# Performance work log

Measured on AMD Instinct MI355X. Metric: run time of the kernel, lower is better.

Reference implementation:

```python
import jax, jax.numpy as jnp
import numpy as np

U = 100000  # num_users
I = 100000  # num_items
D = 64      # dims
L = 50      # seq_L


def setup_inputs() -> dict:
    key = jax.random.key(0)
    ks = jax.random.split(key, 12)
    B, T = 4096, 100
    inp = {
        "user_ids": jax.random.randint(ks[0], (B,), 0, U),
        "item_seq_ids": jax.random.randint(ks[1], (B, L), 0, I),
        "target_item_ids": jax.random.randint(ks[2], (B, T), 0, I),
        # embedding tables (normal init)
        "user_table": jax.random.normal(ks[3], (U, D), jnp.float32) * 0.01,
        "item_table": jax.random.normal(ks[4], (I, D), jnp.float32) * 0.01,
        "W2_table": jax.random.normal(ks[5], (I, D), jnp.float32) * 0.01,
        "b2_table": jnp.zeros((I, 1), jnp.float32),
        # feature gates: Linear(dims, dims), he_uniform weight, zero bias
        "fg_item_W": jax.random.uniform(ks[6], (D, D), jnp.float32, -1.0, 1.0) * np.sqrt(6.0 / D),
        "fg_item_b": jnp.zeros((D,), jnp.float32),
        "fg_user_W": jax.random.uniform(ks[7], (D, D), jnp.float32, -1.0, 1.0) * np.sqrt(6.0 / D),
        "fg_user_b": jnp.zeros((D,), jnp.float32),
        # instance gates: xavier_uniform
        "inst_gate_item": jax.random.uniform(ks[8], (D, 1), jnp.float32, -1.0, 1.0) * np.sqrt(6.0 / (D + 1)),
        "inst_gate_user": jax.random.uniform(ks[9], (D, L), jnp.float32, -1.0, 1.0) * np.sqrt(6.0 / (D + L)),
    }
    return inp


def _forward_user(user_emb, item_embs, fg_item_W, fg_item_b, fg_user_W, fg_user_b,
                  inst_gate_item, inst_gate_user):
    # user_emb: [B,D], item_embs: [B,L,D]
    gate = jax.nn.sigmoid(
        item_embs @ fg_item_W.T + fg_item_b
        + (user_emb @ fg_user_W.T + fg_user_b)[:, None, :]
    )  # [B,L,D]
    gated = item_embs * gate  # [B,L,D]
    term1 = jnp.einsum("bld,d->bl", gated, inst_gate_item[:, 0])
    term2 = user_emb @ inst_gate_user  # [B,L]
    inst = jax.nn.sigmoid(term1 + term2)  # [B,L]
    union = jnp.sum(gated * inst[:, :, None], axis=1)  # [B,D]
    union = union / jnp.sum(inst, axis=1, keepdims=True)
    return union


def reference(user_ids, item_seq_ids, target_item_ids, user_table, item_table,
              W2_table, b2_table, fg_item_W, fg_item_b, fg_user_W, fg_user_b,
              inst_gate_item, inst_gate_user):
    item_embs = item_table[item_seq_ids]      # [B,L,D]
    user_emb = user_table[user_ids]           # [B,D]
    union = _forward_user(user_emb, item_embs, fg_item_W, fg_item_b,
                          fg_user_W, fg_user_b, inst_gate_item, inst_gate_user)
    w2 = W2_table[target_item_ids]            # [B,T,D]
    b2 = b2_table[target_item_ids][..., 0]    # [B,T]
    res = b2 + jnp.einsum("btd,bd->bt", w2, user_emb)
    res = res + jnp.einsum("bd,btd->bt", union, w2)
    # rel_score: bmm(item_embs, w2^T) summed over L == contract item_embs summed over L with w2
    res = res + jnp.einsum("bd,btd->bt", jnp.sum(item_embs, axis=1), w2)
    return res
```

## Files before the change

kernel.cpp:

```cpp
#include <hip/hip_runtime.h>

#define DD 64
#define LL 50
#define NB 4096
#define NT 100

typedef __attribute__((ext_vector_type(8))) __bf16 bf16x8;
typedef __attribute__((ext_vector_type(4))) float f32x4;

__device__ __forceinline__ float sigmoidf_(float x) {
    return 1.0f / (1.0f + __expf(-x));
}
__device__ __forceinline__ unsigned pack_bf16(float hi, float lo) {
    union { float f; unsigned u; } a, b;
    a.f = hi; b.f = lo;
    return ((a.u + 0x8000u) & 0xffff0000u) | ((b.u + 0x8000u) >> 16);
}
__device__ __forceinline__ uint4 cvt8u(const float* f) {
    uint4 r;
    r.x = pack_bf16(f[1], f[0]);
    r.y = pack_bf16(f[3], f[2]);
    r.z = pack_bf16(f[5], f[4]);
    r.w = pack_bf16(f[7], f[6]);
    return r;
}
__device__ __forceinline__ bf16x8 cvt8(const float* f) {
    return __builtin_bit_cast(bf16x8, cvt8u(f));
}
__device__ __forceinline__ void glds16(const float* g, float* l) {
    __builtin_amdgcn_global_load_lds(
        (const __attribute__((address_space(1))) void*)g,
        (__attribute__((address_space(3))) void*)l, 16, 0, 0);
}
__device__ __forceinline__ void glds4(const float* g, float* l) {
    __builtin_amdgcn_global_load_lds(
        (const __attribute__((address_space(1))) void*)g,
        (__attribute__((address_space(3))) void*)l, 4, 0, 0);
}

__global__ __launch_bounds__(64) void k0_user(
    const int* __restrict__ uid_g, const float* __restrict__ user_table,
    const float* __restrict__ Wu, const float* __restrict__ bu,
    const float* __restrict__ bi, const float* __restrict__ igu,
    const float* __restrict__ Wi,
    float* __restrict__ ufg_ws, float* __restrict__ t2_ws,
    unsigned short* __restrict__ wiB_ws)
{
    if (blockIdx.x == 256) {
        const int n = threadIdx.x;
        float tmp[64];
#pragma unroll
        for (int c4 = 0; c4 < 16; c4++)
            *(float4*)&tmp[c4 * 4] = *(const float4*)(Wi + n * DD + c4 * 4);
#pragma unroll
        for (int ch = 0; ch < 8; ch++)
            *(uint4*)(wiB_ws + n * DD + ch * 8) = cvt8u(tmp + ch * 8);
        return;
    }

    const int lane = threadIdx.x;
    const int c = lane & 15, q = lane >> 4;
    const int uid = uid_g[blockIdx.x * 16 + c];
    const float* urow = user_table + (size_t)uid * DD;

    bf16x8 af[2];
#pragma unroll
    for (int kf = 0; kf < 2; kf++) {
        float tmp[8];
        *(float4*)&tmp[0] = *(const float4*)(urow + kf * 32 + q * 8);
        *(float4*)&tmp[4] = *(const float4*)(urow + kf * 32 + q * 8 + 4);
        af[kf] = cvt8(tmp);
    }

#pragma unroll
    for (int ni = 0; ni < 8; ni++) {
        f32x4 a = {0.f, 0.f, 0.f, 0.f};
#pragma unroll
        for (int kf = 0; kf < 2; kf++) {
            const int k0 = kf * 32 + q * 8;
            float tmp[8];
            if (ni < 4) {
                const float* src = Wu + (ni * 16 + c) * DD + k0;
                *(float4*)&tmp[0] = *(const float4*)src;
                *(float4*)&tmp[4] = *(const float4*)(src + 4);
            } else {
                const int l = ni * 16 + c - 64;
#pragma unroll
                for (int j = 0; j < 8; j++)
                    tmp[j] = (l < LL) ? igu[(k0 + j) * LL + l] : 0.f;
            }
            a = __builtin_amdgcn_mfma_f32_16x16x32_bf16(af[kf], cvt8(tmp), a, 0, 0, 0);
        }
        const int n = ni * 16 + c;
#pragma unroll
        for (int reg = 0; reg < 4; reg++) {
            const int bo = blockIdx.x * 16 + q * 4 + reg;
            if (n < DD)           ufg_ws[bo * DD + n] = a[reg] + bu[n] + bi[n];
            else if (n < DD + LL) t2_ws[bo * DD + (n - DD)] = a[reg];
        }
    }
}

__global__ __launch_bounds__(64) void k1_union(
    const int* __restrict__ uid_g, const int* __restrict__ iid_g,
    const float* __restrict__ user_table, const float* __restrict__ item_table,
    const unsigned short* __restrict__ wiB, const float* __restrict__ igi,
    const float* __restrict__ ufg_ws, const float* __restrict__ t2_ws,
    float* __restrict__ v_ws)
{
    const int lane = threadIdx.x;
    const int c = lane & 15, q = lane >> 4;
    const int b = blockIdx.x;

    __shared__ __align__(16) float sE[52 * DD + DD];
    float* sT = sE + 52 * DD;

    const int* iidp = iid_g + b * LL;
    int ids[13];
#pragma unroll
    for (int s = 0; s < 13; s++) {
        const int r = 4 * s + (lane >> 4);
        ids[s] = iidp[r < LL ? r : LL - 1];
    }

#pragma unroll
    for (int s = 0; s < 13; s++) {
        const int r = 4 * s + (lane >> 4);
        const int j = (lane & 15) ^ (r & 7);
        glds16(item_table + (size_t)ids[s] * DD + j * 4, sE + s * 256);
    }
    glds4(t2_ws + b * DD + (lane < LL ? lane : LL - 1), sT);

    bf16x8 wb[4][2];
#pragma unroll
    for (int ni = 0; ni < 4; ni++)
#pragma unroll
        for (int kf = 0; kf < 2; kf++)
            wb[ni][kf] = __builtin_bit_cast(bf16x8,
                *(const uint4*)(wiB + (ni * 16 + c) * DD + kf * 32 + q * 8));

    float ufg4[4], igi4[4];
#pragma unroll
    for (int ni = 0; ni < 4; ni++) {
        ufg4[ni] = ufg_ws[b * DD + ni * 16 + c];
        igi4[ni] = igi[ni * 16 + c];
    }
    const int uid = uid_g[b];
    const float u = user_table[(size_t)uid * DD + lane];

    __syncthreads();

    bf16x8 ea[4][2];
#pragma unroll
    for (int mi = 0; mi < 4; mi++) {
        const int row = mi * 16 + c;
        const int rr = (row < LL) ? row : 0;
        const float* rowp = sE + rr * DD;
        const int s7 = rr & 7;
#pragma unroll
        for (int kf = 0; kf < 2; kf++) {
            float tmp[8];
            const int ch0 = (kf * 8 + 2 * q) ^ s7;
            const int ch1 = (kf * 8 + 2 * q + 1) ^ s7;
            *(float4*)&tmp[0] = *(const float4*)(rowp + ch0 * 4);
            *(float4*)&tmp[4] = *(const float4*)(rowp + ch1 * 4);
            if (row >= LL) {
#pragma unroll
                for (int i = 0; i < 8; i++) tmp[i] = 0.f;
            }
            ea[mi][kf] = cvt8(tmp);
        }
    }

    float unum[4] = {0.f, 0.f, 0.f, 0.f};
    float sip[4]  = {0.f, 0.f, 0.f, 0.f};
    float isum = 0.f;

#pragma unroll
    for (int mi = 0; mi < 4; mi++) {
        f32x4 acc[4];
#pragma unroll
        for (int ni = 0; ni < 4; ni++) {
            f32x4 a = {0.f, 0.f, 0.f, 0.f};
            a = __builtin_amdgcn_mfma_f32_16x16x32_bf16(ea[mi][0], wb[ni][0], a, 0, 0, 0);
            a = __builtin_amdgcn_mfma_f32_16x16x32_bf16(ea[mi][1], wb[ni][1], a, 0, 0, 0);
            acc[ni] = a;
        }
        float gated[4][4], inst_r[4];
#pragma unroll
        for (int reg = 0; reg < 4; reg++) {
            const int l = mi * 16 + q * 4 + reg;
            const int valid = (l < LL);
            const int lr = valid ? l : 0;
            const int s7 = lr & 7;
            float t1 = 0.f;
#pragma unroll
            for (int ni = 0; ni < 4; ni++) {
                const int phys = (4 * ni + (c >> 2)) ^ s7;
                const float ev = sE[lr * DD + phys * 4 + (c & 3)];
                const float e = valid ? ev : 0.f;
                const float g = sigmoidf_(acc[ni][reg] + ufg4[ni]);
                const float gd = e * g;
                gated[reg][ni] = gd;
                t1 += gd * igi4[ni];
                sip[ni] += e;
            }
            t1 += __shfl_xor(t1, 1); t1 += __shfl_xor(t1, 2);
            t1 += __shfl_xor(t1, 4); t1 += __shfl_xor(t1, 8);
            inst_r[reg] = valid ? sigmoidf_(t1 + sT[lr]) : 0.f;
        }
#pragma unroll
        for (int reg = 0; reg < 4; reg++) {
            isum += inst_r[reg];
#pragma unroll
            for (int ni = 0; ni < 4; ni++)
                unum[ni] += gated[reg][ni] * inst_r[reg];
        }
    }

#pragma unroll
    for (int ni = 0; ni < 4; ni++) {
        unum[ni] += __shfl_xor(unum[ni], 16); unum[ni] += __shfl_xor(unum[ni], 32);
        sip[ni]  += __shfl_xor(sip[ni], 16);  sip[ni]  += __shfl_xor(sip[ni], 32);
    }
    isum += __shfl_xor(isum, 16); isum += __shfl_xor(isum, 32);

    const float un = (q == 0) ? unum[0] : (q == 1) ? unum[1] : (q == 2) ? unum[2] : unum[3];
    const float si = (q == 0) ? sip[0]  : (q == 1) ? sip[1]  : (q == 2) ? sip[2]  : sip[3];
    v_ws[b * DD + lane] = u + un / isum + si;
}

__global__ __launch_bounds__(256) void k2_score(
    const int* __restrict__ tgt_g, const float* __restrict__ W2,
    const float* __restrict__ b2, const float* __restrict__ v_ws,
    float* __restrict__ out)
{
    const int b = blockIdx.x;
    const int tid = threadIdx.x;
    __shared__ float sv[DD];
    __shared__ int sids[112];
    __shared__ float sout[112];

    if (tid < DD) sv[tid] = v_ws[b * DD + tid];
    if (tid < 112) {
        const int t = (tid < NT) ? tid : NT - 1;
        sids[tid] = tgt_g[b * NT + t];
    }
    __syncthreads();

    const int j = tid & 15, g = tid >> 4;
    float4 vr = *(const float4*)&sv[j * 4];

    int id[7];
#pragma unroll
    for (int i = 0; i < 7; i++) id[i] = sids[i * 16 + g];
    float4 wv[7];
#pragma unroll
    for (int i = 0; i < 7; i++)
        wv[i] = *(const float4*)(W2 + (size_t)id[i] * DD + j * 4);
    float bb[7];
#pragma unroll
    for (int i = 0; i < 7; i++) bb[i] = b2[id[i]];

#pragma unroll
    for (int i = 0; i < 7; i++) {
        float s = wv[i].x * vr.x + wv[i].y * vr.y + wv[i].z * vr.z + wv[i].w * vr.w;
        s += __shfl_xor(s, 1); s += __shfl_xor(s, 2);
        s += __shfl_xor(s, 4); s += __shfl_xor(s, 8);
        if (j == 0) sout[i * 16 + g] = s + bb[i];
    }
    __syncthreads();
    if (tid < NT) out[b * NT + tid] = sout[tid];
}

extern "C" void kernel_launch(void* const* d_in, const int* in_sizes, int n_in,
                              void* d_out, int out_size, void* d_ws, size_t ws_size,
                              hipStream_t stream)
{
    const int* user_ids        = (const int*)d_in[0];
    const int* item_seq_ids    = (const int*)d_in[1];
    const int* target_item_ids = (const int*)d_in[2];
    const float* user_tab      = (const float*)d_in[3];
    const float* item_tab      = (const float*)d_in[4];
    const float* W2_tab        = (const float*)d_in[5];
    const float* b2_tab        = (const float*)d_in[6];
    const float* fg_item_W     = (const float*)d_in[7];
    const float* fg_item_b     = (const float*)d_in[8];
    const float* fg_user_W     = (const float*)d_in[9];
    const float* fg_user_b     = (const float*)d_in[10];
    const float* igi           = (const float*)d_in[11];
    const float* igu           = (const float*)d_in[12];
    float* out = (float*)d_out;

    float* ufg_ws = (float*)d_ws;
    float* t2_ws  = ufg_ws + NB * DD;
    float* v_ws   = t2_ws + NB * DD;
    unsigned short* wiB_ws = (unsigned short*)(v_ws + NB * DD);

    k0_user<<<257, 64, 0, stream>>>(user_ids, user_tab, fg_user_W, fg_user_b,
                                    fg_item_b, igu, fg_item_W,
                                    ufg_ws, t2_ws, wiB_ws);
    k1_union<<<NB, 64, 0, stream>>>(user_ids, item_seq_ids, user_tab, item_tab,
                                    wiB_ws, igi, ufg_ws, t2_ws, v_ws);
    k2_score<<<NB, 256, 0, stream>>>(target_item_ids, W2_tab, b2_tab, v_ws, out);
}
```

Baseline: 160.5 us.

## Fuse union and scoring kernels, split L rows across four waves

Merges the union kernel and the scoring kernel into one 256-thread block per batch row. Each of the four waves handles a 16-row slice of the item sequence, and partial sums are reduced through shared memory. W2 rows and b2 values are prefetched into LDS with async global-to-LDS loads so they overlap with the gating math. This removes the v_ws round-trip through global memory and one kernel launch. k0 now uses two waves per block. The cost is much higher LDS use per block (about 45KB), which may limit occupancy, plus extra block-level syncs.

```diff
diff --git a/kernel.cpp b/kernel.cpp
--- a/kernel.cpp
+++ b/kernel.cpp
@@ -38,7 +38,7 @@
         (__attribute__((address_space(3))) void*)l, 4, 0, 0);
 }
 
-__global__ __launch_bounds__(64) void k0_user(
+__global__ __launch_bounds__(128) void k0_user(
     const int* __restrict__ uid_g, const float* __restrict__ user_table,
     const float* __restrict__ Wu, const float* __restrict__ bu,
     const float* __restrict__ bi, const float* __restrict__ igu,
@@ -47,6 +47,7 @@
     unsigned short* __restrict__ wiB_ws)
 {
     if (blockIdx.x == 256) {
+        if (threadIdx.x >= 64) return;
         const int n = threadIdx.x;
         float tmp[64];
 #pragma unroll
@@ -58,7 +59,8 @@
         return;
     }
 
-    const int lane = threadIdx.x;
+    const int lane = threadIdx.x & 63;
+    const int wv = threadIdx.x >> 6;
     const int c = lane & 15, q = lane >> 4;
     const int uid = uid_g[blockIdx.x * 16 + c];
     const float* urow = user_table + (size_t)uid * DD;
@@ -73,7 +75,8 @@
     }
 
 #pragma unroll
-    for (int ni = 0; ni < 8; ni++) {
+    for (int ni0 = 0; ni0 < 4; ni0++) {
+        const int ni = wv * 4 + ni0;
         f32x4 a = {0.f, 0.f, 0.f, 0.f};
 #pragma unroll
         for (int kf = 0; kf < 2; kf++) {
@@ -101,35 +104,82 @@
     }
 }
 
-__global__ __launch_bounds__(64) void k1_union(
+__global__ __launch_bounds__(256) void k1_fused(
     const int* __restrict__ uid_g, const int* __restrict__ iid_g,
+    const int* __restrict__ tgt_g,
     const float* __restrict__ user_table, const float* __restrict__ item_table,
+    const float* __restrict__ W2, const float* __restrict__ b2,
     const unsigned short* __restrict__ wiB, const float* __restrict__ igi,
     const float* __restrict__ ufg_ws, const float* __restrict__ t2_ws,
-    float* __restrict__ v_ws)
+    float* __restrict__ out)
 {
-    const int lane = threadIdx.x;
+    const int tid = threadIdx.x;
+    const int lane = tid & 63;
+    const int w = tid >> 6;
     const int c = lane & 15, q = lane >> 4;
     const int b = blockIdx.x;
 
-    __shared__ __align__(16) float sE[52 * DD + DD];
-    float* sT = sE + 52 * DD;
+    __shared__ __align__(16) float sE[52 * DD];
+    __shared__ __align__(16) float sW[112 * DD];
+    __shared__ __align__(16) float sT[DD];
+    __shared__ __align__(16) float sB[128];
+    __shared__ __align__(16) float sU[4 * DD];
+    __shared__ __align__(16) float sS[4 * DD];
+    __shared__ float sI[4];
+    __shared__ __align__(16) float sV[DD];
+    __shared__ float sOut[112];
 
     const int* iidp = iid_g + b * LL;
-    int ids[13];
-#pragma unroll
-    for (int s = 0; s < 13; s++) {
+    const int* tgtp = tgt_g + b * NT;
+
+    int iid3[3];
+#pragma unroll
+    for (int k = 0; k < 3; k++) {
+        const int s = w + 4 * k;
         const int r = 4 * s + (lane >> 4);
-        ids[s] = iidp[r < LL ? r : LL - 1];
-    }
-
-#pragma unroll
-    for (int s = 0; s < 13; s++) {
+        iid3[k] = iidp[r < LL ? r : LL - 1];
+    }
+    int iid12 = 0;
+    if (w == 0) {
+        const int r = 48 + (lane >> 4);
+        iid12 = iidp[r < LL ? r : LL - 1];
+    }
+#pragma unroll
+    for (int k = 0; k < 3; k++) {
+        const int s = w + 4 * k;
         const int r = 4 * s + (lane >> 4);
-        const int j = (lane & 15) ^ (r & 7);
-        glds16(item_table + (size_t)ids[s] * DD + j * 4, sE + s * 256);
-    }
-    glds4(t2_ws + b * DD + (lane < LL ? lane : LL - 1), sT);
+        const int j2 = (lane & 15) ^ (r & 7);
+        glds16(item_table + (size_t)iid3[k] * DD + j2 * 4, sE + s * 256);
+    }
+    if (w == 0) {
+        const int r = 48 + (lane >> 4);
+        const int j2 = (lane & 15) ^ (r & 7);
+        glds16(item_table + (size_t)iid12 * DD + j2 * 4, sE + 12 * 256);
+    }
+
+    int tids6[6];
+#pragma unroll
+    for (int i = 0; i < 6; i++) {
+        const int s2 = w + 4 * i;
+        tids6[i] = tgtp[4 * s2 + (lane >> 4)];
+    }
+    int tid24 = 0;
+    if (w == 0) tid24 = tgtp[96 + (lane >> 4)];
+#pragma unroll
+    for (int i = 0; i < 6; i++) {
+        const int s2 = w + 4 * i;
+        glds16(W2 + (size_t)tids6[i] * DD + (lane & 15) * 4, sW + s2 * 256);
+    }
+    if (w == 0)
+        glds16(W2 + (size_t)tid24 * DD + (lane & 15) * 4, sW + 24 * 256);
+
+    if (w < 2) {
+        const int sl = w * 64 + lane;
+        const int tb = sl < NT ? sl : NT - 1;
+        glds4(b2 + tgtp[tb], sB + w * 64);
+    }
+    if (w == 1)
+        glds4(t2_ws + b * DD + (lane < LL ? lane : LL - 1), sT);
 
     bf16x8 wb[4][2];
 #pragma unroll
@@ -145,15 +195,17 @@
         ufg4[ni] = ufg_ws[b * DD + ni * 16 + c];
         igi4[ni] = igi[ni * 16 + c];
     }
-    const int uid = uid_g[b];
-    const float u = user_table[(size_t)uid * DD + lane];
+    float u = 0.f;
+    if (w == 0) {
+        const int uid = uid_g[b];
+        u = user_table[(size_t)uid * DD + lane];
+    }
 
     __syncthreads();
 
-    bf16x8 ea[4][2];
-#pragma unroll
-    for (int mi = 0; mi < 4; mi++) {
-        const int row = mi * 16 + c;
+    bf16x8 ea[2];
+    {
+        const int row = w * 16 + c;
         const int rr = (row < LL) ? row : 0;
         const float* rowp = sE + rr * DD;
         const int s7 = rr & 7;
@@ -168,28 +220,26 @@
 #pragma unroll
                 for (int i = 0; i < 8; i++) tmp[i] = 0.f;
             }
-            ea[mi][kf] = cvt8(tmp);
+            ea[kf] = cvt8(tmp);
         }
     }
 
     float unum[4] = {0.f, 0.f, 0.f, 0.f};
     float sip[4]  = {0.f, 0.f, 0.f, 0.f};
     float isum = 0.f;
-
-#pragma unroll
-    for (int mi = 0; mi < 4; mi++) {
+    {
         f32x4 acc[4];
 #pragma unroll
         for (int ni = 0; ni < 4; ni++) {
             f32x4 a = {0.f, 0.f, 0.f, 0.f};
-            a = __builtin_amdgcn_mfma_f32_16x16x32_bf16(ea[mi][0], wb[ni][0], a, 0, 0, 0);
-            a = __builtin_amdgcn_mfma_f32_16x16x32_bf16(ea[mi][1], wb[ni][1], a, 0, 0, 0);
+            a = __builtin_amdgcn_mfma_f32_16x16x32_bf16(ea[0], wb[ni][0], a, 0, 0, 0);
+            a = __builtin_amdgcn_mfma_f32_16x16x32_bf16(ea[1], wb[ni][1], a, 0, 0, 0);
             acc[ni] = a;
         }
         float gated[4][4], inst_r[4];
 #pragma unroll
         for (int reg = 0; reg < 4; reg++) {
-            const int l = mi * 16 + q * 4 + reg;
+            const int l = w * 16 + q * 4 + reg;
             const int valid = (l < LL);
             const int lr = valid ? l : 0;
             const int s7 = lr & 7;
@@ -227,50 +277,32 @@
 
     const float un = (q == 0) ? unum[0] : (q == 1) ? unum[1] : (q == 2) ? unum[2] : unum[3];
     const float si = (q == 0) ? sip[0]  : (q == 1) ? sip[1]  : (q == 2) ? sip[2]  : sip[3];
-    v_ws[b * DD + lane] = u + un / isum + si;
-}
-
-__global__ __launch_bounds__(256) void k2_score(
-    const int* __restrict__ tgt_g, const float* __restrict__ W2,
-    const float* __restrict__ b2, const float* __restrict__ v_ws,
-    float* __restrict__ out)
-{
-    const int b = blockIdx.x;
-    const int tid = threadIdx.x;
-    __shared__ float sv[DD];
-    __shared__ int sids[112];
-    __shared__ float sout[112];
-
-    if (tid < DD) sv[tid] = v_ws[b * DD + tid];
-    if (tid < 112) {
-        const int t = (tid < NT) ? tid : NT - 1;
-        sids[tid] = tgt_g[b * NT + t];
-    }
+    sU[w * DD + lane] = un;
+    sS[w * DD + lane] = si;
+    if (lane == 0) sI[w] = isum;
     __syncthreads();
 
-    const int j = tid & 15, g = tid >> 4;
-    float4 vr = *(const float4*)&sv[j * 4];
-
-    int id[7];
-#pragma unroll
-    for (int i = 0; i < 7; i++) id[i] = sids[i * 16 + g];
-    float4 wv[7];
-#pragma unroll
-    for (int i = 0; i < 7; i++)
-        wv[i] = *(const float4*)(W2 + (size_t)id[i] * DD + j * 4);
-    float bb[7];
-#pragma unroll
-    for (int i = 0; i < 7; i++) bb[i] = b2[id[i]];
-
+    if (w == 0) {
+        const float unt = sU[lane] + sU[DD + lane] + sU[2 * DD + lane] + sU[3 * DD + lane];
+        const float sit = sS[lane] + sS[DD + lane] + sS[2 * DD + lane] + sS[3 * DD + lane];
+        const float ist = sI[0] + sI[1] + sI[2] + sI[3];
+        sV[lane] = u + unt / ist + sit;
+    }
+    __syncthreads();
+
+    const int j = tid & 15, gg = tid >> 4;
+    const float4 vr = *(const float4*)&sV[j * 4];
 #pragma unroll
     for (int i = 0; i < 7; i++) {
-        float s = wv[i].x * vr.x + wv[i].y * vr.y + wv[i].z * vr.z + wv[i].w * vr.w;
+        const int ts = i * 16 + gg;
+        const float4 wvv = *(const float4*)&sW[ts * DD + j * 4];
+        float s = wvv.x * vr.x + wvv.y * vr.y + wvv.z * vr.z + wvv.w * vr.w;
         s += __shfl_xor(s, 1); s += __shfl_xor(s, 2);
         s += __shfl_xor(s, 4); s += __shfl_xor(s, 8);
-        if (j == 0) sout[i * 16 + g] = s + bb[i];
+        if (j == 0 && ts < NT) sOut[ts] = s + sB[ts];
     }
     __syncthreads();
-    if (tid < NT) out[b * NT + tid] = sout[tid];
+    if (tid < NT) out[b * NT + tid] = sOut[tid];
 }
 
 extern "C" void kernel_launch(void* const* d_in, const int* in_sizes, int n_in,
@@ -294,13 +326,12 @@
 
     float* ufg_ws = (float*)d_ws;
     float* t2_ws  = ufg_ws + NB * DD;
-    float* v_ws   = t2_ws + NB * DD;
-    unsigned short* wiB_ws = (unsigned short*)(v_ws + NB * DD);
-
-    k0_user<<<257, 64, 0, stream>>>(user_ids, user_tab, fg_user_W, fg_user_b,
-                                    fg_item_b, igu, fg_item_W,
-                                    ufg_ws, t2_ws, wiB_ws);
-    k1_union<<<NB, 64, 0, stream>>>(user_ids, item_seq_ids, user_tab, item_tab,
-                                    wiB_ws, igi, ufg_ws, t2_ws, v_ws);
-    k2_score<<<NB, 256, 0, stream>>>(target_item_ids, W2_tab, b2_tab, v_ws, out);
-}
+    unsigned short* wiB_ws = (unsigned short*)(t2_ws + NB * DD);
+
+    k0_user<<<257, 128, 0, stream>>>(user_ids, user_tab, fg_user_W, fg_user_b,
+                                     fg_item_b, igu, fg_item_W,
+                                     ufg_ws, t2_ws, wiB_ws);
+    k1_fused<<<NB, 256, 0, stream>>>(user_ids, item_seq_ids, target_item_ids,
+                                     user_tab, item_tab, W2_tab, b2_tab,
+                                     wiB_ws, igi, ufg_ws, t2_ws, out);
+}
```

New measurement: 167.9 us. 4.6% more time.
